# Kernel optimization log

Hardware: AMD Instinct MI355X
Metric: run time of the kernel (lower is better)

The kernel has to match this reference:

```python
import jax, jax.numpy as jnp
import numpy as np

D_K = 64


def setup_inputs() -> dict:
    key = jax.random.key(0)
    k1, k2, k3 = jax.random.split(key, 3)
    B, H, S, DK, DV = 2, 16, 2048, 64, 64
    Q = jax.random.normal(k1, (B, H, S, DK), dtype=jnp.float32)
    K = jax.random.normal(k2, (B, H, S, DK), dtype=jnp.float32)
    V = jax.random.normal(k3, (B, H, S, DV), dtype=jnp.float32)
    # causal mask, True = keep (broadcasts over batch/head as in the torch code)
    mask = jnp.tril(jnp.ones((S, S), dtype=bool))
    return {"Q": Q, "K": K, "V": V, "mask": mask}


def reference(Q, K, V, mask):
    # scores[b,h,c,v] = sum_k Q[b,h,c,k] * K[b,h,v,k]
    scores = jnp.einsum('bhck,bhvk->bhcv', Q, K)
    # torch: B = inf at ~mask; scores - B  ->  -inf at masked positions
    scores = jnp.where(mask, scores, -jnp.inf)
    # scale applied AFTER masking, exactly as in the torch forward
    probs = jax.nn.softmax(scores / jnp.sqrt(jnp.float32(D_K)), axis=-1)
    return probs @ V
```

## Files before the change

kernel.cpp:

```cpp
#include <hip/hip_runtime.h>
#include <hip/hip_bf16.h>

#define S_LEN 2048
#define DIM   64
#define NBH   32
#define NQT   32
#define NQB   16
#define TILE_SH 12288
#define WS_NEED ((size_t)NBH * NQT * TILE_SH * sizeof(short))

typedef __attribute__((ext_vector_type(4))) float f32x4;
typedef __attribute__((ext_vector_type(8))) short s16x8;
typedef __attribute__((ext_vector_type(4))) short s16x4;

#define MFMA_B16(A,B,C) __builtin_amdgcn_mfma_f32_16x16x32_bf16(A,B,C,0,0,0)
#define EX2(x) __builtin_amdgcn_exp2f(x)

__device__ __forceinline__ short f2bf(float x){
  union{float f;unsigned u;} v; v.f=x;
  unsigned r = v.u + 0x7FFFu + ((v.u>>16)&1u);
  return (short)(r>>16);
}
__device__ __forceinline__ float bf2f(short s){
  union{float f;unsigned u;} v; v.u=((unsigned)(unsigned short)s)<<16;
  return v.f;
}
__device__ __forceinline__ unsigned packbf(float a, float b){
  __hip_bfloat162 h = __float22bfloat162_rn(make_float2(a, b));
  union { __hip_bfloat162 h; unsigned u; } cv; cv.h = h; return cv.u;
}
__device__ __forceinline__ int swz(int row){
  return (((row&7) ^ ((row>>2)&7)) << 3);
}

__global__ __launch_bounds__(256) void prep_kv(
    const float* __restrict__ K, const float* __restrict__ V, short* __restrict__ W)
{
  __shared__ short Vl[4096];
  const int b  = blockIdx.x;
  const int bh = b >> 5, t = b & 31;
  const float* Kt = K + ((size_t)bh * S_LEN + t * 64) * DIM;
  const float* Vt = V + ((size_t)bh * S_LEN + t * 64) * DIM;
  short* Wt = W + (size_t)b * TILE_SH;
  const int tid = threadIdx.x;

#pragma unroll
  for (int i = 0; i < 2; ++i) {
    const int m = i * 256 + tid;
    const int r = m >> 3, g = m & 7;
    const int c0 = (g << 3) ^ swz(r);
    float x[8];
    *(f32x4*)&x[0] = *(const f32x4*)(Kt + r * DIM + c0);
    *(f32x4*)&x[4] = *(const f32x4*)(Kt + r * DIM + c0 + 4);
    s16x8 hi, lo;
#pragma unroll
    for (int j = 0; j < 8; ++j) {
      short h = f2bf(x[j]);
      hi[j] = h;
      lo[j] = f2bf(x[j] - bf2f(h));
    }
    *(s16x8*)&Wt[m * 8]        = hi;
    *(s16x8*)&Wt[4096 + m * 8] = lo;
  }

  {
    const int r = tid >> 2;
    const int cb = (tid & 3) << 4;
    float x[16];
#pragma unroll
    for (int q = 0; q < 4; ++q)
      *(f32x4*)&x[q * 4] = *(const f32x4*)(Vt + r * DIM + cb + q * 4);
#pragma unroll
    for (int j = 0; j < 16; ++j) {
      const int c = cb + j;
      Vl[c * 64 + (r ^ swz(c))] = f2bf(x[j]);
    }
  }
  __syncthreads();
#pragma unroll
  for (int i = 0; i < 2; ++i) {
    const int p = (i * 256 + tid) * 8;
    *(s16x8*)&Wt[8192 + p] = *(const s16x8*)&Vl[p];
  }
}

__device__ __forceinline__ void stage24(const short* __restrict__ src, short* dst,
                                        int w, int l) {
#pragma unroll
  for (int q = 0; q < 3; ++q) {
    const int off = (q * 8 + w) << 10;
    __builtin_amdgcn_global_load_lds(
        (const __attribute__((address_space(1))) unsigned*)((const char*)src + off + l * 16),
        (__attribute__((address_space(3))) unsigned*)((char*)dst + off),
        16, 0, 0);
  }
}

__global__ __launch_bounds__(512, 2) void fattn_main(
    const float* __restrict__ Qg, float* __restrict__ Og, const short* __restrict__ W)
{
  __shared__ __attribute__((aligned(16))) short buf[2][TILE_SH];

  const int bid = blockIdx.x;
  const int bh = bid & 31;
  const int qt = (NQB - 1) - (bid >> 5);

  const int tid = threadIdx.x;
  const int w = tid >> 6, l = tid & 63;
  const int l15 = l & 15, lg = l >> 4;

  const short* Wb = W + (size_t)bh * NQT * TILE_SH;
  const float* Qb = Qg + (size_t)bh * S_LEN * DIM;
  float*       Ob = Og + (size_t)bh * S_LEN * DIM;

  const int qg = qt * 128 + w * 16 + l15;
  const float SC = 0.125f * 1.44269504088896f;

  s16x8 qh[2], ql[2];
#pragma unroll
  for (int s = 0; s < 2; ++s) {
    const float* qp = Qb + (size_t)qg * DIM + (lg << 3) + s * 32;
    float qv[8];
    *(f32x4*)&qv[0] = *(const f32x4*)qp;
    *(f32x4*)&qv[4] = *(const f32x4*)(qp + 4);
#pragma unroll
    for (int j = 0; j < 8; ++j) {
      short h = f2bf(qv[j]);
      qh[s][j] = h;
      ql[s][j] = f2bf(qv[j] - bf2f(h));
    }
  }

  f32x4 o[4];
#pragma unroll
  for (int d = 0; d < 4; ++d) o[d] = f32x4{0.f,0.f,0.f,0.f};
  float m = -INFINITY, lsum = 0.f;

  const int nt = 2 * qt + 2;
  const int my_nt = nt - (w < 4 ? 1 : 0);
  stage24(Wb, buf[0], w, l);
  __syncthreads();
  int cur = 0;

  const int src0 = l15 + ((lg & 1) << 5);
  const int src1 = src0 + 16;
  const bool hiH = (lg >= 2);

  for (int t = 0; t < nt; ++t) {
    if (t + 1 < nt) stage24(Wb + (size_t)(t + 1) * TILE_SH, buf[cur ^ 1], w, l);

    if (t < my_nt) {
      const short* bK  = buf[cur];
      const short* bKl = bK + 4096;
      const short* bVt = bK + 8192;

      f32x4 acc[4];
#pragma unroll
      for (int f = 0; f < 4; ++f) acc[f] = f32x4{0.f,0.f,0.f,0.f};
#pragma unroll
      for (int f = 0; f < 4; ++f) {
        const int kr = f * 16 + l15;
#pragma unroll
        for (int s = 0; s < 2; ++s) {
          const int dk = (((lg << 3) + (s << 5)) ^ swz(kr));
          s16x8 ah = *(const s16x8*)&bK [kr * DIM + dk];
          s16x8 al = *(const s16x8*)&bKl[kr * DIM + dk];
          acc[f] = MFMA_B16(ah, qh[s], acc[f]);
          acc[f] = MFMA_B16(ah, ql[s], acc[f]);
          acc[f] = MFMA_B16(al, qh[s], acc[f]);
        }
      }

      const bool diag = (t == my_nt - 1);
      const int kv0 = t * 64;
      float pm = -INFINITY;
#pragma unroll
      for (int f = 0; f < 4; ++f)
#pragma unroll
        for (int r = 0; r < 4; ++r) {
          float zz = acc[f][r] * SC;
          if (diag && (kv0 + f * 16 + (lg << 2) + r) > qg) zz = -INFINITY;
          acc[f][r] = zz;
          pm = fmaxf(pm, zz);
        }
      pm = fmaxf(pm, __shfl_xor(pm, 16));
      pm = fmaxf(pm, __shfl_xor(pm, 32));

      if (!__all(pm <= m)) {
        const float mn = fmaxf(m, pm);
        const float al = EX2(m - mn);
        m = mn; lsum *= al;
#pragma unroll
        for (int d = 0; d < 4; ++d) o[d] *= al;
      }
      float rs = 0.f;
#pragma unroll
      for (int f = 0; f < 4; ++f)
#pragma unroll
        for (int r = 0; r < 4; ++r) {
          const float pv = EX2(acc[f][r] - m);
          acc[f][r] = pv;
          rs += pv;
        }
      rs += __shfl_xor(rs, 16);
      rs += __shfl_xor(rs, 32);
      lsum += rs;

      unsigned U[4][2];
#pragma unroll
      for (int f = 0; f < 4; ++f) {
        U[f][0] = packbf(acc[f][0], acc[f][1]);
        U[f][1] = packbf(acc[f][2], acc[f][3]);
      }
#pragma unroll
      for (int s = 0; s < 2; ++s) {
        unsigned a0 = __shfl(U[2*s][0], src0), a1 = __shfl(U[2*s+1][0], src0);
        unsigned b0 = __shfl(U[2*s][1], src0), b1 = __shfl(U[2*s+1][1], src0);
        unsigned c0 = __shfl(U[2*s][0], src1), c1 = __shfl(U[2*s+1][0], src1);
        unsigned d0 = __shfl(U[2*s][1], src1), d1 = __shfl(U[2*s+1][1], src1);
        union { unsigned u[4]; s16x8 v; } pb;
        pb.u[0] = hiH ? a1 : a0;
        pb.u[1] = hiH ? b1 : b0;
        pb.u[2] = hiH ? c1 : c0;
        pb.u[3] = hiH ? d1 : d0;
        const int kv8 = (lg << 3) + (s << 5);
#pragma unroll
        for (int d = 0; d < 4; ++d) {
          const int dv = d * 16 + l15;
          s16x8 vf = *(const s16x8*)&bVt[dv * DIM + (kv8 ^ swz(dv))];
          o[d] = MFMA_B16(vf, pb.v, o[d]);
        }
      }
    }

    __syncthreads();
    cur ^= 1;
  }

  const float inv = 1.0f / lsum;
#pragma unroll
  for (int d = 0; d < 4; ++d) {
    f32x4 ov;
#pragma unroll
    for (int r = 0; r < 4; ++r) ov[r] = o[d][r] * inv;
    *(f32x4*)(Ob + (size_t)qg * DIM + d * 16 + (lg << 2)) = ov;
  }
}

#define QBLK  64
#define KVBLK 64
#define NPAIR (NQT/2)
#define NBLK  (NBH*NPAIR)

__global__ __launch_bounds__(256) void fattn_fb(
    const float* __restrict__ Qg, const float* __restrict__ Kg,
    const float* __restrict__ Vg, float* __restrict__ Og)
{
  __shared__ __attribute__((aligned(16))) short Khi[KVBLK*DIM];
  __shared__ __attribute__((aligned(16))) short Klo[KVBLK*DIM];
  __shared__ __attribute__((aligned(16))) short Vt [DIM*KVBLK];
  __shared__ __attribute__((aligned(16))) short Pl [4*16*KVBLK];

  int bid0 = blockIdx.x;
  int bid  = (bid0 & 7) * (NBLK/8) + (bid0 >> 3);
  int bh   = bid / NPAIR;
  int pr   = bid % NPAIR;
  const int tid = threadIdx.x;
  const int w = tid >> 6, l = tid & 63, l15 = l & 15, lg = l >> 4;
  const float* Qb = Qg + (size_t)bh * S_LEN * DIM;
  const float* Kb = Kg + (size_t)bh * S_LEN * DIM;
  const float* Vb = Vg + (size_t)bh * S_LEN * DIM;
  float*       Ob = Og + (size_t)bh * S_LEN * DIM;
  const float SC = 0.125f * 1.44269504088896f;

  for (int half = 0; half < 2; ++half) {
    const int qt = half ? (NQT - 1 - pr) : pr;
    const int qg = qt * QBLK + w * 16 + l15;
    s16x8 qh[2], ql[2];
#pragma unroll
    for (int s = 0; s < 2; ++s) {
      const float* qp = Qb + (size_t)qg * DIM + (lg << 3) + s * 32;
      float qv[8];
      *(f32x4*)&qv[0] = *(const f32x4*)qp;
      *(f32x4*)&qv[4] = *(const f32x4*)(qp + 4);
#pragma unroll
      for (int j = 0; j < 8; ++j) {
        short h = f2bf(qv[j]); qh[s][j] = h; ql[s][j] = f2bf(qv[j] - bf2f(h));
      }
    }
    f32x4 o[4];
#pragma unroll
    for (int d = 0; d < 4; ++d) o[d] = f32x4{0.f,0.f,0.f,0.f};
    float m = -INFINITY, lsum = 0.f;
    const int ntiles = qt + 1;
    for (int t = 0; t < ntiles; ++t) {
      const int kv0 = t * KVBLK;
      __syncthreads();
      {
        const int row = tid >> 4, c4 = (tid & 15) << 2;
#pragma unroll
        for (int i = 0; i < 4; ++i) {
          const int r = row + (i << 4);
          const f32x4 kv4 = *(const f32x4*)(Kb + (size_t)(kv0 + r) * DIM + c4);
          const f32x4 vv4 = *(const f32x4*)(Vb + (size_t)(kv0 + r) * DIM + c4);
          const int cs = c4 ^ swz(r);
          s16x4 kh, kl;
#pragma unroll
          for (int j = 0; j < 4; ++j) { short h = f2bf(kv4[j]); kh[j] = h; kl[j] = f2bf(kv4[j] - bf2f(h)); }
          *(s16x4*)&Khi[r * DIM + cs] = kh;
          *(s16x4*)&Klo[r * DIM + cs] = kl;
#pragma unroll
          for (int j = 0; j < 4; ++j) { const int dv = c4 + j; Vt[dv * KVBLK + (r ^ swz(dv))] = f2bf(vv4[j]); }
        }
      }
      __syncthreads();
      f32x4 acc[4];
#pragma unroll
      for (int f = 0; f < 4; ++f) acc[f] = f32x4{0.f,0.f,0.f,0.f};
#pragma unroll
      for (int f = 0; f < 4; ++f) {
        const int kr = f * 16 + l15;
#pragma unroll
        for (int s = 0; s < 2; ++s) {
          const int dk = (((lg << 3) + (s << 5)) ^ swz(kr));
          s16x8 ah = *(const s16x8*)&Khi[kr * DIM + dk];
          s16x8 al = *(const s16x8*)&Klo[kr * DIM + dk];
          acc[f] = MFMA_B16(ah, qh[s], acc[f]);
          acc[f] = MFMA_B16(ah, ql[s], acc[f]);
          acc[f] = MFMA_B16(al, qh[s], acc[f]);
        }
      }
      const bool diag = (t == qt);
      float z[4][4];
#pragma unroll
      for (int f = 0; f < 4; ++f)
#pragma unroll
        for (int r = 0; r < 4; ++r) {
          float zz = acc[f][r] * SC;
          if (diag && (kv0 + f * 16 + (lg << 2) + r) > qg) zz = -INFINITY;
          z[f][r] = zz;
        }
      float pm = z[0][0];
#pragma unroll
      for (int f = 0; f < 4; ++f)
#pragma unroll
        for (int r = 0; r < 4; ++r) pm = fmaxf(pm, z[f][r]);
      pm = fmaxf(pm, __shfl_xor(pm, 16));
      pm = fmaxf(pm, __shfl_xor(pm, 32));
      const float mn = fmaxf(m, pm);
      const float alpha = EX2(m - mn);
      float p[4][4]; float rs = 0.f;
#pragma unroll
      for (int f = 0; f < 4; ++f)
#pragma unroll
        for (int r = 0; r < 4; ++r) { const float pv = EX2(z[f][r] - mn); p[f][r] = pv; rs += pv; }
      rs += __shfl_xor(rs, 16);
      rs += __shfl_xor(rs, 32);
      lsum = lsum * alpha + rs;
      m = mn;
#pragma unroll
      for (int d = 0; d < 4; ++d) o[d] *= alpha;
      short* Pw = &Pl[w * 16 * KVBLK];
#pragma unroll
      for (int f = 0; f < 4; ++f) {
        s16x4 pk;
#pragma unroll
        for (int r = 0; r < 4; ++r) pk[r] = f2bf(p[f][r]);
        const int kvc = (f * 16 + (lg << 2)) ^ swz(l15);
        *(s16x4*)&Pw[l15 * KVBLK + kvc] = pk;
      }
#pragma unroll
      for (int s = 0; s < 2; ++s) {
        const int kv8 = (lg << 3) + s * 32;
        s16x8 pf = *(const s16x8*)&Pw[l15 * KVBLK + (kv8 ^ swz(l15))];
#pragma unroll
        for (int d = 0; d < 4; ++d) {
          const int dv = d * 16 + l15;
          s16x8 vf = *(const s16x8*)&Vt[dv * KVBLK + (kv8 ^ swz(dv))];
          o[d] = MFMA_B16(vf, pf, o[d]);
        }
      }
    }
    const float inv = 1.0f / lsum;
#pragma unroll
    for (int d = 0; d < 4; ++d) {
      f32x4 ov;
#pragma unroll
      for (int r = 0; r < 4; ++r) ov[r] = o[d][r] * inv;
      *(f32x4*)(Ob + (size_t)qg * DIM + d * 16 + (lg << 2)) = ov;
    }
  }
}

extern "C" void kernel_launch(void* const* d_in, const int* in_sizes, int n_in,
                              void* d_out, int out_size, void* d_ws, size_t ws_size,
                              hipStream_t stream) {
  const float* Q = (const float*)d_in[0];
  const float* K = (const float*)d_in[1];
  const float* V = (const float*)d_in[2];
  float* O = (float*)d_out;
  if (ws_size >= WS_NEED) {
    short* W = (short*)d_ws;
    prep_kv  <<<dim3(NBH * NQT), dim3(256), 0, stream>>>(K, V, W);
    fattn_main<<<dim3(NBH * NQB), dim3(512), 0, stream>>>(Q, O, W);
  } else {
    fattn_fb<<<dim3(NBLK), dim3(256), 0, stream>>>(Q, K, V, O);
  }
}
```

Baseline: 167.1 us.

## Software-pipeline QK and PV across a triple-buffered KV ring

The main loop is restructured so the QK^T MFMAs for the next KV tile run alongside the softmax update and PV MFMAs for the current tile. A third LDS buffer is added so two tiles can be prefetched ahead. Launch bounds are raised to 4 blocks per CU, and the V transpose in the prep kernel now writes packed bf16 pairs. In exchange, LDS per block grows, the tighter register budget may cause spills, and warps no longer skip the fully masked last tile.

```diff
diff --git a/kernel.cpp b/kernel.cpp
--- a/kernel.cpp
+++ b/kernel.cpp
@@ -64,16 +64,18 @@
   }
 
   {
-    const int r = tid >> 2;
-    const int cb = (tid & 3) << 4;
-    float x[16];
-#pragma unroll
-    for (int q = 0; q < 4; ++q)
-      *(f32x4*)&x[q * 4] = *(const f32x4*)(Vt + r * DIM + cb + q * 4);
-#pragma unroll
-    for (int j = 0; j < 16; ++j) {
+    const int r2 = (tid >> 3) << 1;
+    const int cb = (tid & 7) << 3;
+    float x0[8], x1[8];
+    *(f32x4*)&x0[0] = *(const f32x4*)(Vt + r2 * DIM + cb);
+    *(f32x4*)&x0[4] = *(const f32x4*)(Vt + r2 * DIM + cb + 4);
+    *(f32x4*)&x1[0] = *(const f32x4*)(Vt + (r2 + 1) * DIM + cb);
+    *(f32x4*)&x1[4] = *(const f32x4*)(Vt + (r2 + 1) * DIM + cb + 4);
+#pragma unroll
+    for (int j = 0; j < 8; ++j) {
       const int c = cb + j;
-      Vl[c * 64 + (r ^ swz(c))] = f2bf(x[j]);
+      const int y = r2 ^ swz(c);
+      ((unsigned*)Vl)[(c * 64 + y) >> 1] = packbf(x0[j], x1[j]);
     }
   }
   __syncthreads();
@@ -96,10 +98,100 @@
   }
 }
 
-__global__ __launch_bounds__(512, 2) void fattn_main(
+__device__ __forceinline__ void qk_tile(f32x4 acc[4], const short* __restrict__ bK,
+                                        const s16x8 qh[2], const s16x8 ql[2],
+                                        int l15, int lg)
+{
+  const short* bKl = bK + 4096;
+#pragma unroll
+  for (int f = 0; f < 4; ++f) acc[f] = f32x4{0.f,0.f,0.f,0.f};
+#pragma unroll
+  for (int f = 0; f < 4; ++f) {
+    const int kr = f * 16 + l15;
+#pragma unroll
+    for (int s = 0; s < 2; ++s) {
+      const int dk = (((lg << 3) + (s << 5)) ^ swz(kr));
+      s16x8 ah = *(const s16x8*)&bK [kr * DIM + dk];
+      s16x8 al = *(const s16x8*)&bKl[kr * DIM + dk];
+      acc[f] = MFMA_B16(ah, qh[s], acc[f]);
+      acc[f] = MFMA_B16(ah, ql[s], acc[f]);
+      acc[f] = MFMA_B16(al, qh[s], acc[f]);
+    }
+  }
+}
+
+__device__ __forceinline__ void sm_update(f32x4 acc[4], f32x4 o[4], float& m, float& lsum,
+                                          int kv0, int qg, int lg, float SC)
+{
+  const bool anymask = (kv0 + 63 > qg);
+  float pm = -INFINITY;
+#pragma unroll
+  for (int f = 0; f < 4; ++f)
+#pragma unroll
+    for (int r = 0; r < 4; ++r) {
+      float zz = acc[f][r] * SC;
+      if (anymask && (kv0 + f * 16 + (lg << 2) + r) > qg) zz = -INFINITY;
+      acc[f][r] = zz;
+      pm = fmaxf(pm, zz);
+    }
+  pm = fmaxf(pm, __shfl_xor(pm, 16));
+  pm = fmaxf(pm, __shfl_xor(pm, 32));
+  if (!__all(pm <= m)) {
+    const float mn = fmaxf(m, pm);
+    const float al = EX2(m - mn);
+    m = mn; lsum *= al;
+#pragma unroll
+    for (int d = 0; d < 4; ++d) o[d] *= al;
+  }
+  float rs = 0.f;
+#pragma unroll
+  for (int f = 0; f < 4; ++f)
+#pragma unroll
+    for (int r = 0; r < 4; ++r) {
+      const float pv = EX2(acc[f][r] - m);
+      acc[f][r] = pv;
+      rs += pv;
+    }
+  rs += __shfl_xor(rs, 16);
+  rs += __shfl_xor(rs, 32);
+  lsum += rs;
+}
+
+__device__ __forceinline__ void pv_tile(const f32x4 p[4], f32x4 o[4],
+                                        const short* __restrict__ bVt,
+                                        int l15, int lg, int src0, int src1, bool hiH)
+{
+  unsigned U[4][2];
+#pragma unroll
+  for (int f = 0; f < 4; ++f) {
+    U[f][0] = packbf(p[f][0], p[f][1]);
+    U[f][1] = packbf(p[f][2], p[f][3]);
+  }
+#pragma unroll
+  for (int s = 0; s < 2; ++s) {
+    unsigned a0 = __shfl(U[2*s][0], src0), a1 = __shfl(U[2*s+1][0], src0);
+    unsigned b0 = __shfl(U[2*s][1], src0), b1 = __shfl(U[2*s+1][1], src0);
+    unsigned c0 = __shfl(U[2*s][0], src1), c1 = __shfl(U[2*s+1][0], src1);
+    unsigned d0 = __shfl(U[2*s][1], src1), d1 = __shfl(U[2*s+1][1], src1);
+    union { unsigned u[4]; s16x8 v; } pb;
+    pb.u[0] = hiH ? a1 : a0;
+    pb.u[1] = hiH ? b1 : b0;
+    pb.u[2] = hiH ? c1 : c0;
+    pb.u[3] = hiH ? d1 : d0;
+    const int kv8 = (lg << 3) + (s << 5);
+#pragma unroll
+    for (int d = 0; d < 4; ++d) {
+      const int dv = d * 16 + l15;
+      s16x8 vf = *(const s16x8*)&bVt[dv * DIM + (kv8 ^ swz(dv))];
+      o[d] = MFMA_B16(vf, pb.v, o[d]);
+    }
+  }
+}
+
+__global__ __launch_bounds__(512, 4) void fattn_main(
     const float* __restrict__ Qg, float* __restrict__ Og, const short* __restrict__ W)
 {
-  __shared__ __attribute__((aligned(16))) short buf[2][TILE_SH];
+  __shared__ __attribute__((aligned(16))) short buf[3][TILE_SH];
 
   const int bid = blockIdx.x;
   const int bh = bid & 31;
@@ -136,106 +228,35 @@
   for (int d = 0; d < 4; ++d) o[d] = f32x4{0.f,0.f,0.f,0.f};
   float m = -INFINITY, lsum = 0.f;
 
-  const int nt = 2 * qt + 2;
-  const int my_nt = nt - (w < 4 ? 1 : 0);
-  stage24(Wb, buf[0], w, l);
-  __syncthreads();
-  int cur = 0;
-
   const int src0 = l15 + ((lg & 1) << 5);
   const int src1 = src0 + 16;
   const bool hiH = (lg >= 2);
 
-  for (int t = 0; t < nt; ++t) {
-    if (t + 1 < nt) stage24(Wb + (size_t)(t + 1) * TILE_SH, buf[cur ^ 1], w, l);
-
-    if (t < my_nt) {
-      const short* bK  = buf[cur];
-      const short* bKl = bK + 4096;
-      const short* bVt = bK + 8192;
-
-      f32x4 acc[4];
-#pragma unroll
-      for (int f = 0; f < 4; ++f) acc[f] = f32x4{0.f,0.f,0.f,0.f};
-#pragma unroll
-      for (int f = 0; f < 4; ++f) {
-        const int kr = f * 16 + l15;
-#pragma unroll
-        for (int s = 0; s < 2; ++s) {
-          const int dk = (((lg << 3) + (s << 5)) ^ swz(kr));
-          s16x8 ah = *(const s16x8*)&bK [kr * DIM + dk];
-          s16x8 al = *(const s16x8*)&bKl[kr * DIM + dk];
-          acc[f] = MFMA_B16(ah, qh[s], acc[f]);
-          acc[f] = MFMA_B16(ah, ql[s], acc[f]);
-          acc[f] = MFMA_B16(al, qh[s], acc[f]);
-        }
-      }
-
-      const bool diag = (t == my_nt - 1);
-      const int kv0 = t * 64;
-      float pm = -INFINITY;
-#pragma unroll
-      for (int f = 0; f < 4; ++f)
-#pragma unroll
-        for (int r = 0; r < 4; ++r) {
-          float zz = acc[f][r] * SC;
-          if (diag && (kv0 + f * 16 + (lg << 2) + r) > qg) zz = -INFINITY;
-          acc[f][r] = zz;
-          pm = fmaxf(pm, zz);
-        }
-      pm = fmaxf(pm, __shfl_xor(pm, 16));
-      pm = fmaxf(pm, __shfl_xor(pm, 32));
-
-      if (!__all(pm <= m)) {
-        const float mn = fmaxf(m, pm);
-        const float al = EX2(m - mn);
-        m = mn; lsum *= al;
-#pragma unroll
-        for (int d = 0; d < 4; ++d) o[d] *= al;
-      }
-      float rs = 0.f;
-#pragma unroll
-      for (int f = 0; f < 4; ++f)
-#pragma unroll
-        for (int r = 0; r < 4; ++r) {
-          const float pv = EX2(acc[f][r] - m);
-          acc[f][r] = pv;
-          rs += pv;
-        }
-      rs += __shfl_xor(rs, 16);
-      rs += __shfl_xor(rs, 32);
-      lsum += rs;
-
-      unsigned U[4][2];
-#pragma unroll
-      for (int f = 0; f < 4; ++f) {
-        U[f][0] = packbf(acc[f][0], acc[f][1]);
-        U[f][1] = packbf(acc[f][2], acc[f][3]);
-      }
-#pragma unroll
-      for (int s = 0; s < 2; ++s) {
-        unsigned a0 = __shfl(U[2*s][0], src0), a1 = __shfl(U[2*s+1][0], src0);
-        unsigned b0 = __shfl(U[2*s][1], src0), b1 = __shfl(U[2*s+1][1], src0);
-        unsigned c0 = __shfl(U[2*s][0], src1), c1 = __shfl(U[2*s+1][0], src1);
-        unsigned d0 = __shfl(U[2*s][1], src1), d1 = __shfl(U[2*s+1][1], src1);
-        union { unsigned u[4]; s16x8 v; } pb;
-        pb.u[0] = hiH ? a1 : a0;
-        pb.u[1] = hiH ? b1 : b0;
-        pb.u[2] = hiH ? c1 : c0;
-        pb.u[3] = hiH ? d1 : d0;
-        const int kv8 = (lg << 3) + (s << 5);
-#pragma unroll
-        for (int d = 0; d < 4; ++d) {
-          const int dv = d * 16 + l15;
-          s16x8 vf = *(const s16x8*)&bVt[dv * DIM + (kv8 ^ swz(dv))];
-          o[d] = MFMA_B16(vf, pb.v, o[d]);
-        }
-      }
-    }
-
+  const int nt = 2 * qt + 2;
+
+  short* b0 = buf[0];
+  short* b1 = buf[1];
+  short* b2 = buf[2];
+  stage24(Wb, b0, w, l);
+  __syncthreads();
+  stage24(Wb + TILE_SH, b1, w, l);
+  f32x4 acc[4];
+  qk_tile(acc, b0, qh, ql, l15, lg);
+  __syncthreads();
+
+  for (int t = 0; t < nt - 1; ++t) {
+    if (t + 2 < nt) stage24(Wb + (size_t)(t + 2) * TILE_SH, b2, w, l);
+    sm_update(acc, o, m, lsum, t * 64, qg, lg, SC);
+    f32x4 acc2[4];
+    qk_tile(acc2, b1, qh, ql, l15, lg);
+    pv_tile(acc, o, b0 + 8192, l15, lg, src0, src1, hiH);
+#pragma unroll
+    for (int f = 0; f < 4; ++f) acc[f] = acc2[f];
+    short* tmp = b0; b0 = b1; b1 = b2; b2 = tmp;
     __syncthreads();
-    cur ^= 1;
-  }
+  }
+  sm_update(acc, o, m, lsum, (nt - 1) * 64, qg, lg, SC);
+  pv_tile(acc, o, b0 + 8192, l15, lg, src0, src1, hiH);
 
   const float inv = 1.0f / lsum;
 #pragma unroll
```

Result: no change. 166.6 us (-0.3%).
